# Performance work log

Measured on AMD Instinct MI355X. Metric: run time of the kernel, lower is better.

The kernel has to match this reference:

```python
import jax, jax.numpy as jnp
import numpy as np

B, S, DM = 2, 4096, 3584      # batch, seq_len, d_model (Zamba2-7B defaults)
H, DH = 112, 64               # n_heads, head_dim -> inner_dim = 7168
CHUNK = 256                   # chunk_size; S % CHUNK == 0 so no padding
INNER = H * DH


def setup_inputs() -> dict:
    key = jax.random.key(0)
    k1, k2, k3, k4 = jax.random.split(key, 4)
    return {
        "hidden_states": jax.random.normal(k1, (B, S, DM), jnp.float32),
        "W_in": jax.random.normal(k2, (2 * INNER, DM), jnp.float32) * 0.02,
        "W_out": jax.random.normal(k3, (DM, INNER), jnp.float32) * 0.02,
        "A_log": jax.random.normal(k4, (H,), jnp.float32),
    }


def reference(hidden_states, W_in, W_out, A_log):
    b, s, _ = hidden_states.shape
    # in_proj (nn.Linear, no bias): y = x @ W.T -> (b, s, 2*inner)
    xz = hidden_states @ W_in.T
    x, z = xz[..., :INNER], xz[..., INNER:]
    x = x.reshape(b, s, H, DH)

    n_chunks = s // CHUNK
    # (n_chunks, b, chunk, H, DH) for scan over chunks
    x_chunks = x.reshape(b, n_chunks, CHUNK, H, DH).transpose(1, 0, 2, 3, 4)

    A = jnp.exp(-jnp.abs(A_log)).astype(x.dtype).reshape(1, 1, H, 1)

    def step(h, xc):
        # per-position-within-chunk recurrence across chunks
        h = h * A + xc * 0.1
        return h, h

    h0 = jnp.zeros((b, CHUNK, H, DH), dtype=x.dtype)
    _, ys = jax.lax.scan(step, h0, x_chunks)  # (n_chunks, b, chunk, H, DH)

    y = ys.transpose(1, 0, 2, 3, 4).reshape(b, s, INNER)
    y = y * jax.nn.sigmoid(z)  # SiLU-style gate on z branch
    return y @ W_out.T
```

## Files before the change

### kernel.cpp

```cpp
#include <hip/hip_runtime.h>
#include <hip/hip_bf16.h>
#include <cstdint>
#include <cstddef>


typedef __bf16 bf16x8 __attribute__((ext_vector_type(8)));
typedef float f32x4 __attribute__((ext_vector_type(4)));
typedef unsigned short us8 __attribute__((ext_vector_type(8)));

__device__ __forceinline__ unsigned short f2bf(float f) {
  return __builtin_bit_cast(unsigned short, (__bf16)f);
}
__device__ __forceinline__ float bf2f(unsigned short u) {
  return (float)__builtin_bit_cast(__bf16, u);
}

__device__ __forceinline__ void async_lds16(const unsigned short* g, unsigned short* l) {
  __builtin_amdgcn_global_load_lds(
      (__attribute__((address_space(1))) void*)(size_t)(const void*)g,
      (__attribute__((address_space(3))) void*)l,
      16, 0, 0);
}

__global__ __launch_bounds__(256) void cvt_f32_bf16(
    const float* __restrict__ src, unsigned short* __restrict__ dst, int n4) {
  int t = blockIdx.x * 256 + threadIdx.x;
  if (t >= n4) return;
  float4 v = reinterpret_cast<const float4*>(src)[t];
  ushort4 o;
  o.x = f2bf(v.x); o.y = f2bf(v.y); o.z = f2bf(v.z); o.w = f2bf(v.w);
  reinterpret_cast<ushort4*>(dst)[t] = o;
}

template <bool OUT_BF16>
__global__ __launch_bounds__(512, 2) void gemm256(
    const unsigned short* __restrict__ A, const unsigned short* __restrict__ Bm,
    void* __restrict__ Cv, int K, int lda, int ldb, int ldc) {
  __shared__ __align__(16) unsigned short lds[65536];

  const int tid  = threadIdx.x;
  const int lane = tid & 63;
  const int wave = tid >> 6;

  const int nbx  = gridDim.x;
  const int nwg  = nbx * gridDim.y;
  const int orig = blockIdx.y * nbx + blockIdx.x;
  const int swz  = (orig & 7) * (nwg >> 3) + (orig >> 3);
  const int bm   = (swz / nbx) * 256;
  const int bn   = (swz % nbx) * 256;

  const int wm  = wave >> 2;
  const int wn  = wave & 3;
  const int l15 = lane & 15;
  const int kq  = lane >> 4;
  const int swzr = kq ^ ((l15 >> 1) & 3);
  const int aoff = (wm * 128 + l15) * 32 + swzr * 8;
  const int boff = (wn * 64  + l15) * 32 + swzr * 8;

  const int srow = wave * 16 + (lane >> 2);
  const int sg   = (lane & 3) ^ ((lane >> 3) & 3);
  const unsigned short* gAr = A  + (size_t)(bm + srow) * lda + sg * 8;
  const unsigned short* gBr = Bm + (size_t)(bn + srow) * ldb + sg * 8;

  auto STAGE = [&](int t, int mat, int kh) {
    unsigned short* ldst = lds + ((((t & 1) * 2 + mat) * 2 + kh) << 13) + wave * 512;
    const unsigned short* g = (mat ? gBr : gAr) + t * 64 + kh * 32;
    const size_t ldx = mat ? (size_t)ldb : (size_t)lda;
    async_lds16(g, ldst);
    async_lds16(g + 128 * ldx, ldst + 4096);
  };

  f32x4 acc[8][4];
#pragma unroll
  for (int i = 0; i < 8; ++i)
#pragma unroll
    for (int j = 0; j < 4; ++j) acc[i][j] = (f32x4){0.f, 0.f, 0.f, 0.f};

  const int NT = K >> 6;

  STAGE(0, 0, 0); STAGE(0, 1, 0); STAGE(0, 0, 1); STAGE(0, 1, 1);
  if (NT > 1) {
    STAGE(1, 1, 0); STAGE(1, 0, 0); STAGE(1, 1, 1);
    asm volatile("s_waitcnt vmcnt(6)" ::: "memory");
  } else {
    asm volatile("s_waitcnt vmcnt(0)" ::: "memory");
  }
  __builtin_amdgcn_s_barrier();

  for (int t = 0; t < NT; ++t) {
    const unsigned short* Ak0 = lds + (t & 1) * 32768;
    const unsigned short* Ak1 = Ak0 + 8192;
    const unsigned short* Bk0 = Ak0 + 16384;
    const unsigned short* Bk1 = Ak0 + 24576;

    bf16x8 a[4], b[4];

#pragma unroll
    for (int i = 0; i < 4; ++i)
      a[i] = *reinterpret_cast<const bf16x8*>(Ak0 + aoff + i * 512);
#pragma unroll
    for (int j = 0; j < 4; ++j)
      b[j] = *reinterpret_cast<const bf16x8*>(Bk0 + boff + j * 512);
    if (t + 1 < NT) STAGE(t + 1, 0, 1);
    __builtin_amdgcn_s_barrier();
    asm volatile("s_waitcnt lgkmcnt(0)" ::: "memory");
    __builtin_amdgcn_s_setprio(1);
#pragma unroll
    for (int i = 0; i < 4; ++i)
#pragma unroll
      for (int j = 0; j < 4; ++j)
        acc[i][j] = __builtin_amdgcn_mfma_f32_16x16x32_bf16(a[i], b[j], acc[i][j], 0, 0, 0);
    __builtin_amdgcn_s_setprio(0);
    __builtin_amdgcn_s_barrier();

#pragma unroll
    for (int i = 0; i < 4; ++i)
      a[i] = *reinterpret_cast<const bf16x8*>(Ak0 + aoff + 2048 + i * 512);
    if (t + 2 < NT) STAGE(t + 2, 1, 0);
    __builtin_amdgcn_s_barrier();
    asm volatile("s_waitcnt lgkmcnt(0)" ::: "memory");
    __builtin_amdgcn_s_setprio(1);
#pragma unroll
    for (int i = 0; i < 4; ++i)
#pragma unroll
      for (int j = 0; j < 4; ++j)
        acc[4 + i][j] = __builtin_amdgcn_mfma_f32_16x16x32_bf16(a[i], b[j], acc[4 + i][j], 0, 0, 0);
    __builtin_amdgcn_s_setprio(0);
    __builtin_amdgcn_s_barrier();

#pragma unroll
    for (int i = 0; i < 4; ++i)
      a[i] = *reinterpret_cast<const bf16x8*>(Ak1 + aoff + i * 512);
#pragma unroll
    for (int j = 0; j < 4; ++j)
      b[j] = *reinterpret_cast<const bf16x8*>(Bk1 + boff + j * 512);
    if (t + 2 < NT) STAGE(t + 2, 0, 0);
    __builtin_amdgcn_s_barrier();
    asm volatile("s_waitcnt lgkmcnt(0)" ::: "memory");
    __builtin_amdgcn_s_setprio(1);
#pragma unroll
    for (int i = 0; i < 4; ++i)
#pragma unroll
      for (int j = 0; j < 4; ++j)
        acc[i][j] = __builtin_amdgcn_mfma_f32_16x16x32_bf16(a[i], b[j], acc[i][j], 0, 0, 0);
    __builtin_amdgcn_s_setprio(0);
    __builtin_amdgcn_s_barrier();

#pragma unroll
    for (int i = 0; i < 4; ++i)
      a[i] = *reinterpret_cast<const bf16x8*>(Ak1 + aoff + 2048 + i * 512);
    if (t + 2 < NT) STAGE(t + 2, 1, 1);
    __builtin_amdgcn_s_barrier();
    asm volatile("s_waitcnt lgkmcnt(0)" ::: "memory");
    __builtin_amdgcn_s_setprio(1);
#pragma unroll
    for (int i = 0; i < 4; ++i)
#pragma unroll
      for (int j = 0; j < 4; ++j)
        acc[4 + i][j] = __builtin_amdgcn_mfma_f32_16x16x32_bf16(a[i], b[j], acc[4 + i][j], 0, 0, 0);
    __builtin_amdgcn_s_setprio(0);
    if (t == NT - 2)      asm volatile("s_waitcnt vmcnt(0)" ::: "memory");
    else if (t < NT - 2)  asm volatile("s_waitcnt vmcnt(6)" ::: "memory");
    __builtin_amdgcn_s_barrier();
  }

#pragma unroll
  for (int mi = 0; mi < 8; ++mi) {
#pragma unroll
    for (int j = 0; j < 4; ++j) {
      const int col = bn + wn * 64 + j * 16 + l15;
#pragma unroll
      for (int r = 0; r < 4; ++r) {
        const int row = bm + wm * 128 + mi * 16 + kq * 4 + r;
        if (OUT_BF16)
          ((unsigned short*)Cv)[(size_t)row * ldc + col] = f2bf(acc[mi][j][r]);
        else
          ((float*)Cv)[(size_t)row * ldc + col] = acc[mi][j][r];
      }
    }
  }
}

__global__ __launch_bounds__(256) void scan_gate(
    unsigned short* __restrict__ xz, const float* __restrict__ A_log) {
  const int tid = blockIdx.x * 256 + threadIdx.x;
  const int i8 = tid % 896;
  const int rb = tid / 896;
  const int r = rb & 255;
  const int b = rb >> 8;
  const int i = i8 * 8;
  const float Ah = __expf(-fabsf(A_log[i >> 6]));

  float st[8];
#pragma unroll
  for (int j = 0; j < 8; ++j) st[j] = 0.f;

  const size_t base = ((size_t)b * 4096 + r) * 14336 + i;
#pragma unroll
  for (int c = 0; c < 16; ++c) {
    const size_t off = base + (size_t)c * (256 * 14336);
    us8 xr = *reinterpret_cast<const us8*>(xz + off);
    us8 zr = *reinterpret_cast<const us8*>(xz + off + 7168);
    us8 yo;
#pragma unroll
    for (int j = 0; j < 8; ++j) {
      st[j] = st[j] * Ah + 0.1f * bf2f(xr[j]);
      const float zv = bf2f(zr[j]);
      const float sg = 1.f / (1.f + __expf(-zv));
      yo[j] = f2bf(st[j] * sg);
    }
    *reinterpret_cast<us8*>(xz + off) = yo;
  }
}

extern "C" void kernel_launch(void* const* d_in, const int* in_sizes, int n_in,
                              void* d_out, int out_size, void* d_ws, size_t ws_size,
                              hipStream_t stream) {
  const float* hidden = (const float*)d_in[0];
  const float* W_in   = (const float*)d_in[1];
  const float* W_out  = (const float*)d_in[2];
  const float* A_log  = (const float*)d_in[3];

  unsigned short* hid_bf  = (unsigned short*)d_ws;
  unsigned short* win_bf  = hid_bf  + 29360128ull;
  unsigned short* wout_bf = win_bf  + 51380224ull;
  unsigned short* xz      = wout_bf + 25690112ull;

  cvt_f32_bf16<<<29360128 / 4 / 256, 256, 0, stream>>>(hidden, hid_bf, 29360128 / 4);
  cvt_f32_bf16<<<51380224 / 4 / 256, 256, 0, stream>>>(W_in, win_bf, 51380224 / 4);
  cvt_f32_bf16<<<25690112 / 4 / 256, 256, 0, stream>>>(W_out, wout_bf, 25690112 / 4);

  gemm256<true><<<dim3(14336 / 256, 8192 / 256), 512, 0, stream>>>(
      hid_bf, win_bf, xz, 3584, 3584, 3584, 14336);

  scan_gate<<<1792, 256, 0, stream>>>(xz, A_log);

  gemm256<false><<<dim3(3584 / 256, 8192 / 256), 512, 0, stream>>>(
      xz, wout_bf, d_out, 7168, 14336, 7168, 3584);
}
```

Baseline: 1.648 ms.

## Double-buffer LDS fragments in GEMM to overlap reads with MFMA

Restructures the GEMM inner loop to use separate even/odd register fragments for A and B. Each next fragment's LDS reads are issued before the current MFMA block, and the barrier count per K-tile drops from eight to four. The explicit lgkmcnt(0) waits are removed, leaving the compiler to place waits, and the intrinsic barriers are replaced with inline-asm s_barrier. This is meant to hide LDS latency behind matrix math, at the cost of more VGPRs and a reliance on compiler-inserted waits to keep buffer reuse correct across async stage writes.

```diff
diff --git a/kernel.cpp b/kernel.cpp
--- a/kernel.cpp
+++ b/kernel.cpp
@@ -85,7 +85,7 @@
   } else {
     asm volatile("s_waitcnt vmcnt(0)" ::: "memory");
   }
-  __builtin_amdgcn_s_barrier();
+  asm volatile("s_barrier" ::: "memory");
 
   for (int t = 0; t < NT; ++t) {
     const unsigned short* Ak0 = lds + (t & 1) * 32768;
@@ -93,75 +93,68 @@
     const unsigned short* Bk0 = Ak0 + 16384;
     const unsigned short* Bk1 = Ak0 + 24576;
 
-    bf16x8 a[4], b[4];
-
-#pragma unroll
-    for (int i = 0; i < 4; ++i)
-      a[i] = *reinterpret_cast<const bf16x8*>(Ak0 + aoff + i * 512);
+    bf16x8 aE[4], aO[4], bE[4], bO[4];
+
+#pragma unroll
+    for (int i = 0; i < 4; ++i)
+      aE[i] = *reinterpret_cast<const bf16x8*>(Ak0 + aoff + i * 512);
 #pragma unroll
     for (int j = 0; j < 4; ++j)
-      b[j] = *reinterpret_cast<const bf16x8*>(Bk0 + boff + j * 512);
+      bE[j] = *reinterpret_cast<const bf16x8*>(Bk0 + boff + j * 512);
+
     if (t + 1 < NT) STAGE(t + 1, 0, 1);
-    __builtin_amdgcn_s_barrier();
-    asm volatile("s_waitcnt lgkmcnt(0)" ::: "memory");
-    __builtin_amdgcn_s_setprio(1);
-#pragma unroll
-    for (int i = 0; i < 4; ++i)
-#pragma unroll
-      for (int j = 0; j < 4; ++j)
-        acc[i][j] = __builtin_amdgcn_mfma_f32_16x16x32_bf16(a[i], b[j], acc[i][j], 0, 0, 0);
-    __builtin_amdgcn_s_setprio(0);
-    __builtin_amdgcn_s_barrier();
-
-#pragma unroll
-    for (int i = 0; i < 4; ++i)
-      a[i] = *reinterpret_cast<const bf16x8*>(Ak0 + aoff + 2048 + i * 512);
+#pragma unroll
+    for (int i = 0; i < 4; ++i)
+      aO[i] = *reinterpret_cast<const bf16x8*>(Ak0 + aoff + 2048 + i * 512);
+    __builtin_amdgcn_s_setprio(1);
+#pragma unroll
+    for (int i = 0; i < 4; ++i)
+#pragma unroll
+      for (int j = 0; j < 4; ++j)
+        acc[i][j] = __builtin_amdgcn_mfma_f32_16x16x32_bf16(aE[i], bE[j], acc[i][j], 0, 0, 0);
+    __builtin_amdgcn_s_setprio(0);
+    asm volatile("s_barrier" ::: "memory");
+
     if (t + 2 < NT) STAGE(t + 2, 1, 0);
-    __builtin_amdgcn_s_barrier();
-    asm volatile("s_waitcnt lgkmcnt(0)" ::: "memory");
-    __builtin_amdgcn_s_setprio(1);
-#pragma unroll
-    for (int i = 0; i < 4; ++i)
-#pragma unroll
-      for (int j = 0; j < 4; ++j)
-        acc[4 + i][j] = __builtin_amdgcn_mfma_f32_16x16x32_bf16(a[i], b[j], acc[4 + i][j], 0, 0, 0);
-    __builtin_amdgcn_s_setprio(0);
-    __builtin_amdgcn_s_barrier();
-
-#pragma unroll
-    for (int i = 0; i < 4; ++i)
-      a[i] = *reinterpret_cast<const bf16x8*>(Ak1 + aoff + i * 512);
+#pragma unroll
+    for (int i = 0; i < 4; ++i)
+      aE[i] = *reinterpret_cast<const bf16x8*>(Ak1 + aoff + i * 512);
+    __builtin_amdgcn_s_setprio(1);
+#pragma unroll
+    for (int i = 0; i < 4; ++i)
+#pragma unroll
+      for (int j = 0; j < 4; ++j)
+        acc[4 + i][j] = __builtin_amdgcn_mfma_f32_16x16x32_bf16(aO[i], bE[j], acc[4 + i][j], 0, 0, 0);
+    __builtin_amdgcn_s_setprio(0);
+    asm volatile("s_barrier" ::: "memory");
+
+    if (t + 2 < NT) STAGE(t + 2, 0, 0);
 #pragma unroll
     for (int j = 0; j < 4; ++j)
-      b[j] = *reinterpret_cast<const bf16x8*>(Bk1 + boff + j * 512);
-    if (t + 2 < NT) STAGE(t + 2, 0, 0);
-    __builtin_amdgcn_s_barrier();
-    asm volatile("s_waitcnt lgkmcnt(0)" ::: "memory");
-    __builtin_amdgcn_s_setprio(1);
-#pragma unroll
-    for (int i = 0; i < 4; ++i)
-#pragma unroll
-      for (int j = 0; j < 4; ++j)
-        acc[i][j] = __builtin_amdgcn_mfma_f32_16x16x32_bf16(a[i], b[j], acc[i][j], 0, 0, 0);
-    __builtin_amdgcn_s_setprio(0);
-    __builtin_amdgcn_s_barrier();
-
-#pragma unroll
-    for (int i = 0; i < 4; ++i)
-      a[i] = *reinterpret_cast<const bf16x8*>(Ak1 + aoff + 2048 + i * 512);
+      bO[j] = *reinterpret_cast<const bf16x8*>(Bk1 + boff + j * 512);
+#pragma unroll
+    for (int i = 0; i < 4; ++i)
+      aO[i] = *reinterpret_cast<const bf16x8*>(Ak1 + aoff + 2048 + i * 512);
+    __builtin_amdgcn_s_setprio(1);
+#pragma unroll
+    for (int i = 0; i < 4; ++i)
+#pragma unroll
+      for (int j = 0; j < 4; ++j)
+        acc[i][j] = __builtin_amdgcn_mfma_f32_16x16x32_bf16(aE[i], bO[j], acc[i][j], 0, 0, 0);
+    __builtin_amdgcn_s_setprio(0);
+    asm volatile("s_barrier" ::: "memory");
+
     if (t + 2 < NT) STAGE(t + 2, 1, 1);
-    __builtin_amdgcn_s_barrier();
-    asm volatile("s_waitcnt lgkmcnt(0)" ::: "memory");
-    __builtin_amdgcn_s_setprio(1);
-#pragma unroll
-    for (int i = 0; i < 4; ++i)
-#pragma unroll
-      for (int j = 0; j < 4; ++j)
-        acc[4 + i][j] = __builtin_amdgcn_mfma_f32_16x16x32_bf16(a[i], b[j], acc[4 + i][j], 0, 0, 0);
+    __builtin_amdgcn_s_setprio(1);
+#pragma unroll
+    for (int i = 0; i < 4; ++i)
+#pragma unroll
+      for (int j = 0; j < 4; ++j)
+        acc[4 + i][j] = __builtin_amdgcn_mfma_f32_16x16x32_bf16(aO[i], bO[j], acc[4 + i][j], 0, 0, 0);
     __builtin_amdgcn_s_setprio(0);
     if (t == NT - 2)      asm volatile("s_waitcnt vmcnt(0)" ::: "memory");
     else if (t < NT - 2)  asm volatile("s_waitcnt vmcnt(6)" ::: "memory");
-    __builtin_amdgcn_s_barrier();
+    asm volatile("s_barrier" ::: "memory");
   }
 
 #pragma unroll
```

Result: faster. 1.601 ms (-2.8%).
